# Kernel tuning notes

Measured on AMD Instinct MI355X. Metric: run time of the kernel, lower is better.

The kernel has to match this reference:

```python
import jax, jax.numpy as jnp
import numpy as np


def _make_pert(r, s):
    lin = np.linspace(-r, r, s)
    xm, ym, tm = np.meshgrid(lin, lin, lin)  # default 'xy' indexing, matches torch code
    return jnp.asarray(np.stack([xm.ravel(), ym.ravel(), tm.ravel()], axis=-1), dtype=jnp.float32)

PERTS = (_make_pert(0.01, 3), _make_pert(0.05, 5), _make_pert(0.09, 7))  # [27,3],[125,3],[343,3]

N, IN, H, HQ, FF, OUT = 4096, 3, 256, 64, 64, 3


def setup_inputs():
    key = jax.random.key(0)
    ks = jax.random.split(key, 24)

    def W(k, i, o):
        return (jax.random.normal(k, (i, o), jnp.float32) / np.sqrt(i)).astype(jnp.float32)

    one = jnp.ones((1,), jnp.float32)
    return {
        "x": jax.random.normal(ks[0], (N, 1), jnp.float32),
        "y": jax.random.normal(ks[1], (N, 1), jnp.float32),
        "t": jax.random.normal(ks[2], (N, 1), jnp.float32),
        # linear_emb: 3 -> 64 -> WaveAct -> 256
        "emb_W1": W(ks[3], IN, HQ), "emb_b1": jnp.zeros((HQ,), jnp.float32),
        "emb_wa": one, "emb_wb": one,
        "emb_W2": W(ks[4], HQ, H), "emb_b2": jnp.zeros((H,), jnp.float32),
        # multiregion_mixer: 4 -> 8 -> WaveAct -> 1
        "mix_W1": W(ks[5], 4, 8), "mix_b1": jnp.zeros((8,), jnp.float32),
        "mix_wa": one, "mix_wb": one,
        "mix_W2": W(ks[6], 8, 1), "mix_b2": jnp.zeros((1,), jnp.float32),
        "out_W0": W(ks[7], H, FF), "out_b0": jnp.zeros((FF,), jnp.float32),
        "out_wa0": one, "out_wb0": one,
        "out_Wh": jnp.stack([W(ks[8 + i], FF, FF) for i in range(3)]),
        "out_bh": jnp.zeros((3, FF), jnp.float32),
        "out_wah": jnp.ones((3, 1), jnp.float32), "out_wbh": jnp.ones((3, 1), jnp.float32),
        "out_Wf1": W(ks[11], FF, FF), "out_bf1": jnp.zeros((FF,), jnp.float32),
        "out_waf": one, "out_wbf": one,
        "out_Wf2": W(ks[12], FF, OUT), "out_bf2": jnp.zeros((OUT,), jnp.float32),
    }


def _wave(h, wa, wb):
    return wa * jnp.sin(h) + wb * jnp.cos(h)


def reference(x, y, t,
              emb_W1, emb_b1, emb_wa, emb_wb, emb_W2, emb_b2,
              mix_W1, mix_b1, mix_wa, mix_wb, mix_W2, mix_b2,
              out_W0, out_b0, out_wa0, out_wb0,
              out_Wh, out_bh, out_wah, out_wbh,
              out_Wf1, out_bf1, out_waf, out_wbf, out_Wf2, out_bf2):
    def emb(s):  # [..., 3] -> [..., 256]
        h = _wave(s @ emb_W1 + emb_b1, emb_wa, emb_wb)
        return h @ emb_W2 + emb_b2

    src = jnp.concatenate([x, y, t], axis=-1)           # [N, 3]
    feats = [emb(src)]                                   # region 1: unperturbed
    for P in PERTS:
        perturbed = src[:, None, :] + P[None, :, :]      # [N, P, 3]
        feats.append(emb(perturbed).mean(axis=1))        # [N, 256]
    stacked = jnp.stack(feats, axis=-1)                  # [N, 256, 4] (== permute(0,2,1) of stack dim=1)

    m = _wave(stacked @ mix_W1 + mix_b1, mix_wa, mix_wb) # [N, 256, 8]
    e = (m @ mix_W2 + mix_b2)[:, :, 0]                   # [N, 256]

    h = _wave(e @ out_W0 + out_b0, out_wa0, out_wb0)     # [N, 64]
    for i in range(3):                                   # fixed num_layer-1 = 3 hidden layers
        h = _wave(h @ out_Wh[i] + out_bh[i], out_wah[i], out_wbh[i])
    h = _wave(h @ out_Wf1 + out_bf1, out_waf, out_wbf)
    return h @ out_Wf2 + out_bf2                         # [N, 3]
```

## Files before the change

kernel.cpp:

```cpp
#include <hip/hip_runtime.h>

#define SPB 4

__global__ __launch_bounds__(256) void model_fused(
    const float* __restrict__ x, const float* __restrict__ y, const float* __restrict__ t,
    const float* __restrict__ embW1, const float* __restrict__ embb1,
    const float* __restrict__ embwa, const float* __restrict__ embwb,
    const float* __restrict__ embW2, const float* __restrict__ embb2,
    const float* __restrict__ mixW1, const float* __restrict__ mixb1,
    const float* __restrict__ mixwa, const float* __restrict__ mixwb,
    const float* __restrict__ mixW2, const float* __restrict__ mixb2,
    const float* __restrict__ outW0, const float* __restrict__ outb0,
    const float* __restrict__ outwa0, const float* __restrict__ outwb0,
    const float* __restrict__ outWh, const float* __restrict__ outbh,
    const float* __restrict__ outwah, const float* __restrict__ outwbh,
    const float* __restrict__ outWf1, const float* __restrict__ outbf1,
    const float* __restrict__ outwaf, const float* __restrict__ outwbf,
    const float* __restrict__ outWf2, const float* __restrict__ outbf2,
    float* __restrict__ out, int N)
{
    __shared__ float sC[3][64];
    __shared__ float sw[SPB][64];
    __shared__ float se[SPB][256];
    __shared__ float sh[2][SPB][64];
    __shared__ float sMixW1[32], sMixb1[8], sMixW2[8];

    const int tid = threadIdx.x;
    const int n0  = blockIdx.x * SPB;

    if (tid < 32)       sMixW1[tid]      = mixW1[tid];
    else if (tid < 40)  sMixb1[tid - 32] = mixb1[tid - 32];
    else if (tid < 48)  sMixW2[tid - 40] = mixW2[tid - 40];

    {
        const int ch = tid & 63;
        const int sm = tid >> 6;
        const float w0 = embW1[ch], w1 = embW1[64 + ch], w2 = embW1[128 + ch];
        if (sm == 0) {
            float ga = (1.f + 2.f*__cosf(0.01f*w0))
                     * (1.f + 2.f*__cosf(0.01f*w1))
                     * (1.f + 2.f*__cosf(0.01f*w2)) * (1.f/27.f);
            float gb = (1.f + 2.f*(__cosf(0.025f*w0) + __cosf(0.05f*w0)))
                     * (1.f + 2.f*(__cosf(0.025f*w1) + __cosf(0.05f*w1)))
                     * (1.f + 2.f*(__cosf(0.025f*w2) + __cosf(0.05f*w2))) * (1.f/125.f);
            float gc = (1.f + 2.f*(__cosf(0.03f*w0) + __cosf(0.06f*w0) + __cosf(0.09f*w0)))
                     * (1.f + 2.f*(__cosf(0.03f*w1) + __cosf(0.06f*w1) + __cosf(0.09f*w1)))
                     * (1.f + 2.f*(__cosf(0.03f*w2) + __cosf(0.06f*w2) + __cosf(0.09f*w2))) * (1.f/343.f);
            sC[0][ch] = ga; sC[1][ch] = gb; sC[2][ch] = gc;
        }
        const int n  = n0 + sm;
        const int ns = (n < N) ? n : (N - 1);
        float u = x[ns]*w0 + y[ns]*w1 + t[ns]*w2 + embb1[ch];
        sw[sm][ch] = embwa[0]*__sinf(u) + embwb[0]*__cosf(u);
    }
    __syncthreads();

    {
        const int c = tid;
        float a0[SPB], a1[SPB], a2[SPB], a3[SPB];
        #pragma unroll
        for (int n = 0; n < SPB; ++n) { a0[n]=0.f; a1[n]=0.f; a2[n]=0.f; a3[n]=0.f; }

        #pragma unroll 4
        for (int ch = 0; ch < 64; ++ch) {
            const float wr = embW2[ch*256 + c];
            const float c1 = sC[0][ch], c2 = sC[1][ch], c3 = sC[2][ch];
            #pragma unroll
            for (int n = 0; n < SPB; ++n) {
                const float tn = sw[n][ch] * wr;
                a0[n] += tn;
                a1[n] = fmaf(tn, c1, a1[n]);
                a2[n] = fmaf(tn, c2, a2[n]);
                a3[n] = fmaf(tn, c3, a3[n]);
            }
        }

        const float mwa = mixwa[0], mwb = mixwb[0], mb2 = mixb2[0];
        const float bb2 = embb2[c];
        #pragma unroll
        for (int n = 0; n < SPB; ++n) {
            const float s0 = a0[n]+bb2, s1 = a1[n]+bb2, s2 = a2[n]+bb2, s3 = a3[n]+bb2;
            float ev = mb2;
            #pragma unroll
            for (int j = 0; j < 8; ++j) {
                float p = fmaf(s0, sMixW1[j],
                          fmaf(s1, sMixW1[8 + j],
                          fmaf(s2, sMixW1[16 + j],
                          fmaf(s3, sMixW1[24 + j], sMixb1[j]))));
                ev = fmaf(mwa*__sinf(p) + mwb*__cosf(p), sMixW2[j], ev);
            }
            se[n][c] = ev;
        }
    }
    __syncthreads();

    const int n = tid >> 6, f = tid & 63;
    {
        float a = outb0[f];
        for (int k = 0; k < 256; ++k)
            a = fmaf(se[n][k], outW0[k*64 + f], a);
        sh[0][n][f] = outwa0[0]*__sinf(a) + outwb0[0]*__cosf(a);
    }
    __syncthreads();

    int cur = 0;
    #pragma unroll
    for (int i = 0; i < 3; ++i) {
        float a = outbh[i*64 + f];
        const float* W = outWh + i*4096;
        #pragma unroll 8
        for (int k = 0; k < 64; ++k)
            a = fmaf(sh[cur][n][k], W[k*64 + f], a);
        sh[1 - cur][n][f] = outwah[i]*__sinf(a) + outwbh[i]*__cosf(a);
        __syncthreads();
        cur ^= 1;
    }
    {
        float a = outbf1[f];
        #pragma unroll 8
        for (int k = 0; k < 64; ++k)
            a = fmaf(sh[cur][n][k], outWf1[k*64 + f], a);
        sh[1 - cur][n][f] = outwaf[0]*__sinf(a) + outwbf[0]*__cosf(a);
        __syncthreads();
        cur ^= 1;
    }
    if (tid < SPB*3) {
        const int nn = tid / 3, o = tid - nn*3;
        float a = outbf2[o];
        #pragma unroll 8
        for (int k = 0; k < 64; ++k)
            a = fmaf(sh[cur][nn][k], outWf2[k*3 + o], a);
        const int gn = n0 + nn;
        if (gn < N) out[gn*3 + o] = a;
    }
}

extern "C" void kernel_launch(void* const* d_in, const int* in_sizes, int n_in,
                              void* d_out, int out_size, void* d_ws, size_t ws_size,
                              hipStream_t stream) {
    const float* x      = (const float*)d_in[0];
    const float* y      = (const float*)d_in[1];
    const float* t      = (const float*)d_in[2];
    const float* embW1  = (const float*)d_in[3];
    const float* embb1  = (const float*)d_in[4];
    const float* embwa  = (const float*)d_in[5];
    const float* embwb  = (const float*)d_in[6];
    const float* embW2  = (const float*)d_in[7];
    const float* embb2  = (const float*)d_in[8];
    const float* mixW1  = (const float*)d_in[9];
    const float* mixb1  = (const float*)d_in[10];
    const float* mixwa  = (const float*)d_in[11];
    const float* mixwb  = (const float*)d_in[12];
    const float* mixW2  = (const float*)d_in[13];
    const float* mixb2  = (const float*)d_in[14];
    const float* outW0  = (const float*)d_in[15];
    const float* outb0  = (const float*)d_in[16];
    const float* outwa0 = (const float*)d_in[17];
    const float* outwb0 = (const float*)d_in[18];
    const float* outWh  = (const float*)d_in[19];
    const float* outbh  = (const float*)d_in[20];
    const float* outwah = (const float*)d_in[21];
    const float* outwbh = (const float*)d_in[22];
    const float* outWf1 = (const float*)d_in[23];
    const float* outbf1 = (const float*)d_in[24];
    const float* outwaf = (const float*)d_in[25];
    const float* outwbf = (const float*)d_in[26];
    const float* outWf2 = (const float*)d_in[27];
    const float* outbf2 = (const float*)d_in[28];
    float* out = (float*)d_out;

    const int N = in_sizes[0];
    const int blocks = (N + SPB - 1) / SPB;
    model_fused<<<blocks, 256, 0, stream>>>(
        x, y, t,
        embW1, embb1, embwa, embwb, embW2, embb2,
        mixW1, mixb1, mixwa, mixwb, mixW2, mixb2,
        outW0, outb0, outwa0, outwb0,
        outWh, outbh, outwah, outwbh,
        outWf1, outbf1, outwaf, outwbf, outWf2, outbf2,
        out, N);
}
```

Before: 140.5 us.

## Halve samples per block, split-K the 256x64 layer, spread setup trig across warps

Lowers samples per block from 4 to 2, doubling the grid to 2048 blocks and adding a min-blocks launch bound hint for occupancy. The 256-wide output layer is split into two K-halves computed by all 256 threads and reduced through shared memory, and the perturbation-constant trig setup is spread across otherwise-idle thread groups. The cost is that each embW2/outW0 weight load is now reused across only 2 samples instead of 4, and half the threads sit idle in the later 64-wide layers.

```diff
diff --git a/kernel.cpp b/kernel.cpp
--- a/kernel.cpp
+++ b/kernel.cpp
@@ -1,8 +1,8 @@
 #include <hip/hip_runtime.h>
 
-#define SPB 4
-
-__global__ __launch_bounds__(256) void model_fused(
+#define SPB 2
+
+__global__ __launch_bounds__(256, 8) void model_fused(
     const float* __restrict__ x, const float* __restrict__ y, const float* __restrict__ t,
     const float* __restrict__ embW1, const float* __restrict__ embb1,
     const float* __restrict__ embwa, const float* __restrict__ embwb,
@@ -22,6 +22,7 @@
     __shared__ float sC[3][64];
     __shared__ float sw[SPB][64];
     __shared__ float se[SPB][256];
+    __shared__ float pf[2][SPB][64];
     __shared__ float sh[2][SPB][64];
     __shared__ float sMixW1[32], sMixb1[8], sMixW2[8];
 
@@ -36,50 +37,47 @@
         const int ch = tid & 63;
         const int sm = tid >> 6;
         const float w0 = embW1[ch], w1 = embW1[64 + ch], w2 = embW1[128 + ch];
-        if (sm == 0) {
+        if (sm < SPB) {
+            const int n  = n0 + sm;
+            const int ns = (n < N) ? n : (N - 1);
+            float u = x[ns]*w0 + y[ns]*w1 + t[ns]*w2 + embb1[ch];
+            sw[sm][ch] = embwa[0]*__sinf(u) + embwb[0]*__cosf(u);
+        } else if (sm == 2) {
             float ga = (1.f + 2.f*__cosf(0.01f*w0))
                      * (1.f + 2.f*__cosf(0.01f*w1))
                      * (1.f + 2.f*__cosf(0.01f*w2)) * (1.f/27.f);
             float gb = (1.f + 2.f*(__cosf(0.025f*w0) + __cosf(0.05f*w0)))
                      * (1.f + 2.f*(__cosf(0.025f*w1) + __cosf(0.05f*w1)))
                      * (1.f + 2.f*(__cosf(0.025f*w2) + __cosf(0.05f*w2))) * (1.f/125.f);
+            sC[0][ch] = ga; sC[1][ch] = gb;
+        } else {
             float gc = (1.f + 2.f*(__cosf(0.03f*w0) + __cosf(0.06f*w0) + __cosf(0.09f*w0)))
                      * (1.f + 2.f*(__cosf(0.03f*w1) + __cosf(0.06f*w1) + __cosf(0.09f*w1)))
                      * (1.f + 2.f*(__cosf(0.03f*w2) + __cosf(0.06f*w2) + __cosf(0.09f*w2))) * (1.f/343.f);
-            sC[0][ch] = ga; sC[1][ch] = gb; sC[2][ch] = gc;
-        }
-        const int n  = n0 + sm;
-        const int ns = (n < N) ? n : (N - 1);
-        float u = x[ns]*w0 + y[ns]*w1 + t[ns]*w2 + embb1[ch];
-        sw[sm][ch] = embwa[0]*__sinf(u) + embwb[0]*__cosf(u);
+            sC[2][ch] = gc;
+        }
     }
     __syncthreads();
 
     {
         const int c = tid;
-        float a0[SPB], a1[SPB], a2[SPB], a3[SPB];
-        #pragma unroll
-        for (int n = 0; n < SPB; ++n) { a0[n]=0.f; a1[n]=0.f; a2[n]=0.f; a3[n]=0.f; }
-
-        #pragma unroll 4
+        float a00=0.f,a01=0.f,a02=0.f,a03=0.f;
+        float a10=0.f,a11=0.f,a12=0.f,a13=0.f;
+
+        #pragma unroll 8
         for (int ch = 0; ch < 64; ++ch) {
             const float wr = embW2[ch*256 + c];
             const float c1 = sC[0][ch], c2 = sC[1][ch], c3 = sC[2][ch];
-            #pragma unroll
-            for (int n = 0; n < SPB; ++n) {
-                const float tn = sw[n][ch] * wr;
-                a0[n] += tn;
-                a1[n] = fmaf(tn, c1, a1[n]);
-                a2[n] = fmaf(tn, c2, a2[n]);
-                a3[n] = fmaf(tn, c3, a3[n]);
-            }
+            const float t0 = sw[0][ch] * wr;
+            const float t1 = sw[1][ch] * wr;
+            a00 += t0; a01 = fmaf(t0, c1, a01); a02 = fmaf(t0, c2, a02); a03 = fmaf(t0, c3, a03);
+            a10 += t1; a11 = fmaf(t1, c1, a11); a12 = fmaf(t1, c2, a12); a13 = fmaf(t1, c3, a13);
         }
 
         const float mwa = mixwa[0], mwb = mixwb[0], mb2 = mixb2[0];
         const float bb2 = embb2[c];
-        #pragma unroll
-        for (int n = 0; n < SPB; ++n) {
-            const float s0 = a0[n]+bb2, s1 = a1[n]+bb2, s2 = a2[n]+bb2, s3 = a3[n]+bb2;
+        {
+            const float s0 = a00+bb2, s1 = a01+bb2, s2 = a02+bb2, s3 = a03+bb2;
             float ev = mb2;
             #pragma unroll
             for (int j = 0; j < 8; ++j) {
@@ -89,16 +87,40 @@
                           fmaf(s3, sMixW1[24 + j], sMixb1[j]))));
                 ev = fmaf(mwa*__sinf(p) + mwb*__cosf(p), sMixW2[j], ev);
             }
-            se[n][c] = ev;
-        }
-    }
-    __syncthreads();
-
-    const int n = tid >> 6, f = tid & 63;
+            se[0][c] = ev;
+        }
+        {
+            const float s0 = a10+bb2, s1 = a11+bb2, s2 = a12+bb2, s3 = a13+bb2;
+            float ev = mb2;
+            #pragma unroll
+            for (int j = 0; j < 8; ++j) {
+                float p = fmaf(s0, sMixW1[j],
+                          fmaf(s1, sMixW1[8 + j],
+                          fmaf(s2, sMixW1[16 + j],
+                          fmaf(s3, sMixW1[24 + j], sMixb1[j]))));
+                ev = fmaf(mwa*__sinf(p) + mwb*__cosf(p), sMixW2[j], ev);
+            }
+            se[1][c] = ev;
+        }
+    }
+    __syncthreads();
+
     {
-        float a = outb0[f];
-        for (int k = 0; k < 256; ++k)
-            a = fmaf(se[n][k], outW0[k*64 + f], a);
+        const int h = tid >> 7;
+        const int r = tid & 127;
+        const int n = r >> 6, f = r & 63;
+        const int k0 = h * 128;
+        float p = 0.f;
+        #pragma unroll 8
+        for (int k = 0; k < 128; ++k)
+            p = fmaf(se[n][k0 + k], outW0[(k0 + k)*64 + f], p);
+        pf[h][n][f] = p;
+    }
+    __syncthreads();
+
+    const int n = (tid >> 6) & 1, f = tid & 63;
+    if (tid < 128) {
+        float a = pf[0][n][f] + pf[1][n][f] + outb0[f];
         sh[0][n][f] = outwa0[0]*__sinf(a) + outwb0[0]*__cosf(a);
     }
     __syncthreads();
@@ -106,24 +128,27 @@
     int cur = 0;
     #pragma unroll
     for (int i = 0; i < 3; ++i) {
-        float a = outbh[i*64 + f];
-        const float* W = outWh + i*4096;
-        #pragma unroll 8
-        for (int k = 0; k < 64; ++k)
-            a = fmaf(sh[cur][n][k], W[k*64 + f], a);
-        sh[1 - cur][n][f] = outwah[i]*__sinf(a) + outwbh[i]*__cosf(a);
+        if (tid < 128) {
+            float a = outbh[i*64 + f];
+            const float* W = outWh + i*4096;
+            #pragma unroll 8
+            for (int k = 0; k < 64; ++k)
+                a = fmaf(sh[cur][n][k], W[k*64 + f], a);
+            sh[1 - cur][n][f] = outwah[i]*__sinf(a) + outwbh[i]*__cosf(a);
+        }
         __syncthreads();
         cur ^= 1;
     }
-    {
+    if (tid < 128) {
         float a = outbf1[f];
         #pragma unroll 8
         for (int k = 0; k < 64; ++k)
             a = fmaf(sh[cur][n][k], outWf1[k*64 + f], a);
         sh[1 - cur][n][f] = outwaf[0]*__sinf(a) + outwbf[0]*__cosf(a);
-        __syncthreads();
-        cur ^= 1;
-    }
+    }
+    __syncthreads();
+    cur ^= 1;
+
     if (tid < SPB*3) {
         const int nn = tid / 3, o = tid - nn*3;
         float a = outbf2[o];
```

After: 146.8 us. +4.5%, slower.
